# Kernel tuning notes

Measured on AMD Instinct MI355X. Metric: run time of the kernel, lower is better.

## Reference

```python
import math
import jax, jax.numpy as jnp
import numpy as np

THETA = 2 ** 16

def _get_freqs(n: int) -> jnp.ndarray:
    # positions quantized to multiples of 2 (pairs share a frequency)
    pos = jnp.floor(jnp.arange(n, dtype=jnp.float32) / 2.0) * 2.0
    return 1.0 / (THETA ** (pos / n)) / (2.0 * math.pi)  # (n,)

def _rope(phases: jnp.ndarray, v: jnp.ndarray) -> jnp.ndarray:
    # phases in 'cycles'; wrap to [0,1) then scale to radians
    ph = (phases % 1.0) * (2.0 * math.pi)
    c, s = jnp.cos(ph), jnp.sin(ph)
    # interleaved rotate-half: out[..., 2i] = -v[..., 2i+1], out[..., 2i+1] = v[..., 2i]
    v_rot = jnp.stack((-v[..., 1::2], v[..., ::2]), axis=-1).reshape(v.shape)
    return (v * c).astype(v.dtype) + (v_rot * s).astype(v.dtype)


def setup_inputs() -> dict:
    key = jax.random.key(0)
    kq, kv = jax.random.split(key)
    B, H, T, N, D = 2, 8, 2048, 1024, 128
    Q = jax.random.normal(kq, (B, H, T, N), dtype=jnp.float32)
    K = Q  # module asserts K is Q
    V = jax.random.normal(kv, (B, H, T, D), dtype=jnp.float32)
    return {"Q": Q, "K": K, "V": V}


def reference(Q, K, V):
    B, H, T, N = Q.shape
    freqs = _get_freqs(N)  # (N,)
    # r_phases: (T, N) = position * freq (broadcast over B, H)
    r_phases = jnp.arange(T, dtype=jnp.float32)[:, None] * freqs[None, :]
    QR = _rope(r_phases, Q)  # (B,H,T,N); KR = QR since K is Q
    scores = jnp.einsum('bhtn,bhsn->bhts', QR, QR)  # (B,H,T,T)
    causal = jnp.tril(jnp.ones((T, T), dtype=bool), k=-1)  # strict lower triangle
    scores = jnp.where(causal, scores, 0.0)
    return jnp.einsum('bhts,bhsd->bhtd', scores, V)  # (B,H,T,D)
```

## Files before the change

### kernel.cpp

```cpp
#include <hip/hip_runtime.h>

typedef __bf16 bf16_t;
typedef bf16_t bf16x8 __attribute__((ext_vector_type(8)));
typedef float f32x4 __attribute__((ext_vector_type(4)));
typedef unsigned short u16;
typedef unsigned int u32;

#define T_DIM 2048
#define N_DIM 1024
#define D_DIM 128

__device__ __forceinline__ u16 f32_to_bf16(float f) {
    u32 u = __builtin_bit_cast(u32, f);
    u += 0x7FFFu + ((u >> 16) & 1u);
    return (u16)(u >> 16);
}
__device__ __forceinline__ float bf16_to_f32(u16 v) {
    u32 u = (u32)v << 16;
    return __builtin_bit_cast(float, u);
}

typedef __attribute__((address_space(1))) const u32 guint;
typedef __attribute__((address_space(3))) u32 luint;
__device__ __forceinline__ void stage16(const void* g, void* l) {
    __builtin_amdgcn_global_load_lds((guint*)g, (luint*)l, 16, 0, 0);
}
__device__ __forceinline__ void wait_vm0_barrier() {
    asm volatile("s_waitcnt vmcnt(0)" ::: "memory");
    __builtin_amdgcn_s_barrier();
}

__global__ void ropet_kernel(const float* __restrict__ Q, u16* __restrict__ QR,
                             u16* __restrict__ QRt) {
    __shared__ __align__(16) u16 til[64][136];
    const int bh  = blockIdx.x >> 8;
    const int rem = blockIdx.x & 255;
    const int t0 = (rem >> 3) * 64, n0 = (rem & 7) * 128;
    const float* src = Q + (size_t)bh * ((size_t)T_DIM * N_DIM) + (size_t)t0 * N_DIM + n0;
    u16* qdst = QR + (size_t)bh * ((size_t)T_DIM * N_DIM) + (size_t)t0 * N_DIM + n0;
    #pragma unroll
    for (int k = 0; k < 4; ++k) {
        const int slot = k * 256 + threadIdx.x;
        const int r  = slot >> 4;
        const int f8 = slot & 15;
        const float4 qa = *(const float4*)(src + (size_t)r * N_DIM + f8 * 8);
        const float4 qb = *(const float4*)(src + (size_t)r * N_DIM + f8 * 8 + 4);
        const float vin[4][2] = {{qa.x, qa.y}, {qa.z, qa.w}, {qb.x, qb.y}, {qb.z, qb.w}};
        const int t = t0 + r;
        u16 ov[8];
        #pragma unroll
        for (int pp = 0; pp < 4; ++pp) {
            const int pidx = (n0 >> 1) + f8 * 4 + pp;
            const float freq = exp2f((float)pidx * (-1.0f / 32.0f)) * 0.15915494309189535f;
            float ph = (float)t * freq;
            ph -= floorf(ph);
            const float s = __builtin_amdgcn_sinf(ph);
            const float c = __builtin_amdgcn_cosf(ph);
            ov[2 * pp]     = f32_to_bf16(vin[pp][0] * c - vin[pp][1] * s);
            ov[2 * pp + 1] = f32_to_bf16(vin[pp][1] * c + vin[pp][0] * s);
        }
        *(uint4*)(qdst + (size_t)r * N_DIM + f8 * 8) = *(const uint4*)ov;
        *(uint4*)(&til[r][(f8 * 8) ^ (((r >> 3) & 7) << 3)]) = *(const uint4*)ov;
    }
    __syncthreads();
    u16* tdst = QRt + (size_t)bh * ((size_t)N_DIM * T_DIM) + (size_t)n0 * T_DIM + t0;
    #pragma unroll
    for (int k = 0; k < 4; ++k) {
        const int slot = k * 256 + threadIdx.x;
        const int nl = slot >> 3;
        const int t8 = slot & 7;
        u16 ov2[8];
        #pragma unroll
        for (int e = 0; e < 8; ++e)
            ov2[e] = til[t8 * 8 + e][nl ^ (t8 << 3)];
        *(uint4*)(tdst + (size_t)nl * T_DIM + t8 * 8) = *(const uint4*)ov2;
    }
}

__global__ void vt_kernel(const float* __restrict__ V, u16* __restrict__ Vt) {
    __shared__ u16 tile[64][65];
    const int bh   = blockIdx.x >> 6;
    const int rem  = blockIdx.x & 63;
    const int t0 = (rem >> 1) * 64, d0 = (rem & 1) * 64;
    const float* src = V + ((size_t)bh * T_DIM + t0) * D_DIM + d0;
    #pragma unroll
    for (int k = 0; k < 16; ++k) {
        int linear = k * 256 + threadIdx.x;
        int r = linear >> 6, c = linear & 63;
        tile[r][c] = f32_to_bf16(src[(size_t)r * D_DIM + c]);
    }
    __syncthreads();
    u16* dst = Vt + ((size_t)bh * D_DIM + d0) * T_DIM + t0;
    #pragma unroll
    for (int k = 0; k < 16; ++k) {
        int linear = k * 256 + threadIdx.x;
        int dr = linear >> 6, tc = linear & 63;
        dst[(size_t)dr * T_DIM + tc] = tile[tc][dr];
    }
}

__global__ __launch_bounds__(512, 2)
void statescan_kernel(const u16* __restrict__ QRt, const u16* __restrict__ Vt,
                      u16* __restrict__ UP) {
    __shared__ __align__(16) u16 Smem[24576];

    const int b  = blockIdx.x;
    const int bh = b >> 4;
    const int nt = (b >> 1) & 7;
    const int dt = b & 1;

    const int tid  = threadIdx.x;
    const int w    = tid >> 6;
    const int wy   = w >> 1, wx = w & 1;
    const int lane = tid & 63;
    const int quad = lane >> 4;
    const int l15  = lane & 15;
    const int sw   = l15 & 7;
    const int srow = lane >> 3;
    const int scol = (lane & 7) ^ (srow & 7);

    const u16* Ag = Vt  + (size_t)bh * ((size_t)D_DIM * T_DIM) + (size_t)(dt * 64)  * T_DIM;
    const u16* Bg = QRt + (size_t)bh * ((size_t)N_DIM * T_DIM) + (size_t)(nt * 128) * T_DIM;

    const f32x4 fz = {0.f, 0.f, 0.f, 0.f};
    f32x4 acc[4];
    #pragma unroll
    for (int nj = 0; nj < 4; ++nj) acc[nj] = fz;

    auto STAGE = [&](int buf, int s) {
        const int toff = s * 64;
        if (w < 4) {
            #pragma unroll
            for (int ia = 0; ia < 2; ++ia)
                stage16(Ag + (size_t)(w * 16 + ia * 8 + srow) * T_DIM + toff + scol * 8,
                        Smem + buf * 4096 + (w * 16 + ia * 8) * 64);
        }
        #pragma unroll
        for (int ib = 0; ib < 2; ++ib)
            stage16(Bg + (size_t)(w * 16 + ib * 8 + srow) * T_DIM + toff + scol * 8,
                    Smem + 8192 + buf * 8192 + (w * 16 + ib * 8) * 64);
    };

    u16* upb = UP + (size_t)(bh * 16) * (128 * (size_t)N_DIM)
                  + (size_t)(dt * 64) * N_DIM + nt * 128;

    auto WRITE_UP = [&](int ci) {
        u16* ub = upb + (size_t)ci * (128 * (size_t)N_DIM);
        #pragma unroll
        for (int nj = 0; nj < 4; ++nj)
            #pragma unroll
            for (int rr = 0; rr < 4; ++rr)
                ub[(size_t)(wy * 16 + quad * 4 + rr) * N_DIM + wx * 64 + nj * 16 + l15]
                    = f32_to_bf16(acc[nj][rr]);
    };

    STAGE(0, 0);
    wait_vm0_barrier();
    int buf = 0;
    for (int s = 0; s < 30; ++s) {
        if ((s & 1) == 0) WRITE_UP(s >> 1);
        if (s < 29) STAGE(buf ^ 1, s + 1);
        const char* As = (const char*)(Smem + buf * 4096);
        const char* Bs = (const char*)(Smem + 8192 + buf * 8192);
        #pragma unroll
        for (int kc = 0; kc < 2; ++kc) {
            bf16x8 af, bfr[4];
            af = *(const bf16x8*)(As + (wy * 16 + l15) * 128 + (((kc * 4 + quad) ^ sw) << 4));
            #pragma unroll
            for (int nj = 0; nj < 4; ++nj)
                bfr[nj] = *(const bf16x8*)(Bs + (wx * 64 + nj * 16 + l15) * 128 + (((kc * 4 + quad) ^ sw) << 4));
            #pragma unroll
            for (int nj = 0; nj < 4; ++nj)
                acc[nj] = __builtin_amdgcn_mfma_f32_16x16x32_bf16(af, bfr[nj], acc[nj], 0, 0, 0);
        }
        wait_vm0_barrier();
        buf ^= 1;
    }
    WRITE_UP(15);
}

__global__ __launch_bounds__(512, 2)
void attn3_kernel(const u16* __restrict__ QR, const u16* __restrict__ UP,
                  const u16* __restrict__ Vt, float* __restrict__ Out) {
    __shared__ __align__(16) u16 Smem[32768];
    u16 (*Ps)[140] = (u16 (*)[140])Smem;

    const int b  = (blockIdx.x & 7) * 32 + (blockIdx.x >> 3);
    const int bh = b >> 4;
    const int i  = b & 15;

    const int tid  = threadIdx.x;
    const int w    = tid >> 6;
    const int wy   = w >> 1, wx = w & 1;
    const int lane = tid & 63;
    const int quad = lane >> 4;
    const int l15  = lane & 15;
    const int sw   = l15 & 7;
    const int srow = lane >> 3;
    const int scol = (lane & 7) ^ (srow & 7);

    const u16* Ap = QR + (size_t)bh * ((size_t)T_DIM * N_DIM)
                       + (size_t)(i * 128 + w * 16 + srow) * N_DIM + scol * 8;
    const u16* Bp = UP + (size_t)(b * 128 + w * 16 + srow) * N_DIM + scol * 8;

    const f32x4 fz = {0.f, 0.f, 0.f, 0.f};
    f32x4 sm[2][4], si[2][4];
    #pragma unroll
    for (int mi = 0; mi < 2; ++mi)
        #pragma unroll
        for (int nj = 0; nj < 4; ++nj) {
            sm[mi][nj] = fz;
            si[mi][nj] = fz;
        }

    auto STAGE = [&](int buf, int kk16) {
        const int kk = kk16 * 64;
        #pragma unroll
        for (int ii = 0; ii < 2; ++ii) {
            stage16(Ap + (size_t)(ii * 8) * N_DIM + kk, Smem + buf * 8192 + (w * 16 + ii * 8) * 64);
            stage16(Bp + (size_t)(ii * 8) * N_DIM + kk, Smem + 16384 + buf * 8192 + (w * 16 + ii * 8) * 64);
        }
    };

    STAGE(0, 0);
    wait_vm0_barrier();
    int buf = 0;
    for (int kk16 = 0; kk16 < 16; ++kk16) {
        if (kk16 < 15) STAGE(buf ^ 1, kk16 + 1);
        const char* As = (const char*)(Smem + buf * 8192);
        const char* Bs = (const char*)(Smem + 16384 + buf * 8192);
        #pragma unroll
        for (int kc = 0; kc < 2; ++kc) {
            bf16x8 af[2], bm[4], bi[4];
            #pragma unroll
            for (int mi = 0; mi < 2; ++mi)
                af[mi] = *(const bf16x8*)(As + (wy * 32 + mi * 16 + l15) * 128 + (((kc * 4 + quad) ^ sw) << 4));
            #pragma unroll
            for (int nj = 0; nj < 4; ++nj) {
                bm[nj] = *(const bf16x8*)(Bs + (wx * 64 + nj * 16 + l15) * 128 + (((kc * 4 + quad) ^ sw) << 4));
                bi[nj] = *(const bf16x8*)(As + (wx * 64 + nj * 16 + l15) * 128 + (((kc * 4 + quad) ^ sw) << 4));
            }
            #pragma unroll
            for (int mi = 0; mi < 2; ++mi)
                #pragma unroll
                for (int nj = 0; nj < 4; ++nj) {
                    sm[mi][nj] = __builtin_amdgcn_mfma_f32_16x16x32_bf16(af[mi], bm[nj], sm[mi][nj], 0, 0, 0);
                    si[mi][nj] = __builtin_amdgcn_mfma_f32_16x16x32_bf16(af[mi], bi[nj], si[mi][nj], 0, 0, 0);
                }
        }
        wait_vm0_barrier();
        buf ^= 1;
    }

    #pragma unroll
    for (int mi = 0; mi < 2; ++mi) {
        const int rowb = wy * 32 + mi * 16 + quad * 4;
        #pragma unroll
        for (int nj = 0; nj < 4; ++nj) {
            const int col = wx * 64 + nj * 16 + l15;
            #pragma unroll
            for (int rr = 0; rr < 4; ++rr)
                if (col >= rowb + rr) si[mi][nj][rr] = 0.f;
        }
    }
    #pragma unroll
    for (int mi = 0; mi < 2; ++mi) {
        const int rowb = wy * 32 + mi * 16 + quad * 4;
        #pragma unroll
        for (int nj = 0; nj < 4; ++nj) {
            const int col = wx * 64 + nj * 16 + l15;
            #pragma unroll
            for (int rr = 0; rr < 4; ++rr)
                Ps[rowb + rr][col] = f32_to_bf16(si[mi][nj][rr]);
        }
    }
    __syncthreads();

    const u16* vjb = Vt + (size_t)bh * ((size_t)D_DIM * T_DIM)
                        + (size_t)(wx * 64 + l15) * T_DIM + i * 128 + quad * 8;
    #pragma unroll
    for (int kc = 0; kc < 4; ++kc) {
        bf16x8 pf[2];
        #pragma unroll
        for (int mi = 0; mi < 2; ++mi)
            pf[mi] = *(const bf16x8*)(&Ps[wy * 32 + mi * 16 + l15][kc * 32 + quad * 8]);
        #pragma unroll
        for (int nj = 0; nj < 4; ++nj) {
            const bf16x8 vv = *(const bf16x8*)(vjb + (size_t)(nj * 16) * T_DIM + kc * 32);
            #pragma unroll
            for (int mi = 0; mi < 2; ++mi)
                sm[mi][nj] = __builtin_amdgcn_mfma_f32_16x16x32_bf16(pf[mi], vv, sm[mi][nj], 0, 0, 0);
        }
    }

    float* ob = Out + ((size_t)bh * T_DIM + (size_t)i * 128) * D_DIM;
    #pragma unroll
    for (int mi = 0; mi < 2; ++mi)
        #pragma unroll
        for (int nj = 0; nj < 4; ++nj)
            #pragma unroll
            for (int rr = 0; rr < 4; ++rr)
                ob[(size_t)(wy * 32 + mi * 16 + quad * 4 + rr) * D_DIM + wx * 64 + nj * 16 + l15]
                    = sm[mi][nj][rr];
}

__global__ void rope_kernel(const float* __restrict__ Q, u16* __restrict__ QR) {
    const int g = blockIdx.x * 256 + threadIdx.x;
    const int base = g * 4;
    const int t  = (base >> 9) & (T_DIM - 1);
    const int p0 = base & 511;
    const float4 qa = ((const float4*)Q)[g * 2];
    const float4 qb = ((const float4*)Q)[g * 2 + 1];
    const float vin[4][2] = {{qa.x, qa.y}, {qa.z, qa.w}, {qb.x, qb.y}, {qb.z, qb.w}};
    u16 ov[8];
    #pragma unroll
    for (int uu = 0; uu < 4; ++uu) {
        const float freq = exp2f((float)(p0 + uu) * (-1.0f / 32.0f)) * 0.15915494309189535f;
        float ph = (float)t * freq;
        ph = ph - floorf(ph);
        const float s = __builtin_amdgcn_sinf(ph);
        const float c = __builtin_amdgcn_cosf(ph);
        ov[2 * uu]     = f32_to_bf16(vin[uu][0] * c - vin[uu][1] * s);
        ov[2 * uu + 1] = f32_to_bf16(vin[uu][1] * c + vin[uu][0] * s);
    }
    ((uint4*)QR)[g] = *(const uint4*)ov;
}

__device__ __forceinline__ int run_start(int b) { return b < 128 ? 5 * b : 640 + 4 * (b - 128); }

__global__ __launch_bounds__(256, 2)
void attn_kernel(const u16* __restrict__ QR, const u16* __restrict__ Vt,
                 float* __restrict__ Out, u16* __restrict__ Part) {
    __shared__ __align__(16) u16 Smem[17920];
    u16 (*As)[64]  = (u16 (*)[64])Smem;
    u16 (*Bs)[64]  = (u16 (*)[64])(Smem + 8192);
    u16 (*Ps)[140] = (u16 (*)[140])Smem;

    const int b     = blockIdx.x;
    const int start = run_start(b);
    const int len   = b < 128 ? 5 : 4;

    const int tid  = threadIdx.x;
    const int w    = tid >> 6;
    const int wy   = w >> 1, wx = w & 1;
    const int lane = tid & 63;
    const int quad = lane >> 4;
    const int l15  = lane & 15;
    const int sw   = l15 & 7;
    const int srow = lane >> 3;
    const int scol = (lane & 7) ^ (srow & 7);

    const f32x4 fz = {0.f, 0.f, 0.f, 0.f};
    f32x4 o_acc[4][4];
    int cur_bh = -1, cur_qt = -1;
    bool hasj0 = false;
    const u16* QRb = QR;
    const u16* Ap  = QR;
    const u16* Vb  = Vt;

    for (int it = 0; it < len; ++it) {
        const int i = start + it;
        const int bh = i / 136;
        const int r  = i - bh * 136;
        int qt = 15, j = 0, acc = 0;
        #pragma unroll 1
        for (int q = 0; q < 16; ++q) {
            if (r < acc + q + 1) { qt = q; j = r - acc; break; }
            acc += q + 1;
        }

        if (qt != cur_qt || bh != cur_bh) {
            if (cur_qt >= 0) {
                if (hasj0) {
                    float* ob = Out + ((size_t)cur_bh * T_DIM + (size_t)cur_qt * 128) * D_DIM;
                    #pragma unroll
                    for (int mi = 0; mi < 4; ++mi)
                        #pragma unroll
                        for (int nj = 0; nj < 4; ++nj)
                            #pragma unroll
                            for (int rr = 0; rr < 4; ++rr)
                                ob[(size_t)(wy * 64 + mi * 16 + quad * 4 + rr) * D_DIM + wx * 64 + nj * 16 + l15] = o_acc[mi][nj][rr];
                } else {
                    u16* pb = Part + (size_t)b * 16384;
                    #pragma unroll
                    for (int mi = 0; mi < 4; ++mi)
                        #pragma unroll
                        for (int nj = 0; nj < 4; ++nj)
                            #pragma unroll
                            for (int rr = 0; rr < 4; ++rr)
                                pb[(wy * 64 + mi * 16 + quad * 4 + rr) * 128 + wx * 64 + nj * 16 + l15] = f32_to_bf16(o_acc[mi][nj][rr]);
                }
            }
            cur_bh = bh; cur_qt = qt; hasj0 = (j == 0);
            #pragma unroll
            for (int mi = 0; mi < 4; ++mi)
                #pragma unroll
                for (int nj = 0; nj < 4; ++nj)
                    o_acc[mi][nj] = fz;
            QRb = QR + (size_t)bh * (T_DIM * N_DIM);
            Ap  = QRb + (size_t)(qt * 128 + w * 32 + srow) * N_DIM + scol * 8;
            Vb  = Vt + (size_t)bh * (D_DIM * T_DIM) + (size_t)(wx * 64 + l15) * T_DIM + quad * 8;
        }

        const u16* Bp = QRb + (size_t)(j * 128 + w * 32 + srow) * N_DIM + scol * 8;
        f32x4 s_acc[4][4];
        #pragma unroll
        for (int mi = 0; mi < 4; ++mi)
            #pragma unroll
            for (int nj = 0; nj < 4; ++nj)
                s_acc[mi][nj] = fz;

        __syncthreads();

        for (int kk = 0; kk < N_DIM; kk += 64) {
            #pragma unroll
            for (int ii = 0; ii < 4; ++ii) {
                stage16(Ap + (size_t)ii * 8 * N_DIM + kk, &As[w * 32 + ii * 8][0]);
                stage16(Bp + (size_t)ii * 8 * N_DIM + kk, &Bs[w * 32 + ii * 8][0]);
            }
            __syncthreads();
            #pragma unroll
            for (int kc = 0; kc < 2; ++kc) {
                bf16x8 af[4], bfr[4];
                #pragma unroll
                for (int mi = 0; mi < 4; ++mi)
                    af[mi] = *(const bf16x8*)((const char*)As + (wy * 64 + mi * 16 + l15) * 128 + (((kc * 4 + quad) ^ sw) << 4));
                #pragma unroll
                for (int nj = 0; nj < 4; ++nj)
                    bfr[nj] = *(const bf16x8*)((const char*)Bs + (wx * 64 + nj * 16 + l15) * 128 + (((kc * 4 + quad) ^ sw) << 4));
                #pragma unroll
                for (int mi = 0; mi < 4; ++mi)
                    #pragma unroll
                    for (int nj = 0; nj < 4; ++nj)
                        s_acc[mi][nj] = __builtin_amdgcn_mfma_f32_16x16x32_bf16(af[mi], bfr[nj], s_acc[mi][nj], 0, 0, 0);
            }
            __syncthreads();
        }

        if (j == qt) {
            #pragma unroll
            for (int mi = 0; mi < 4; ++mi) {
                const int rowb = wy * 64 + mi * 16 + quad * 4;
                #pragma unroll
                for (int nj = 0; nj < 4; ++nj) {
                    const int col = wx * 64 + nj * 16 + l15;
                    #pragma unroll
                    for (int rr = 0; rr < 4; ++rr)
                        if (col >= rowb + rr) s_acc[mi][nj][rr] = 0.f;
                }
            }
        }

        #pragma unroll
        for (int mi = 0; mi < 4; ++mi) {
            const int rowb = wy * 64 + mi * 16 + quad * 4;
            #pragma unroll
            for (int nj = 0; nj < 4; ++nj) {
                const int col = wx * 64 + nj * 16 + l15;
                #pragma unroll
                for (int rr = 0; rr < 4; ++rr)
                    Ps[rowb + rr][col] = f32_to_bf16(s_acc[mi][nj][rr]);
            }
        }
        __syncthreads();

        const u16* vjb = Vb + j * 128;
        #pragma unroll
        for (int kc = 0; kc < 4; ++kc) {
            bf16x8 pf[4];
            #pragma unroll
            for (int mi = 0; mi < 4; ++mi)
                pf[mi] = *(const bf16x8*)(&Ps[wy * 64 + mi * 16 + l15][kc * 32 + quad * 8]);
            #pragma unroll
            for (int nj = 0; nj < 4; ++nj) {
                const bf16x8 vv = *(const bf16x8*)(vjb + (size_t)(nj * 16) * T_DIM + kc * 32);
                #pragma unroll
                for (int mi = 0; mi < 4; ++mi)
                    o_acc[mi][nj] = __builtin_amdgcn_mfma_f32_16x16x32_bf16(pf[mi], vv, o_acc[mi][nj], 0, 0, 0);
            }
        }
    }

    if (hasj0) {
        float* ob = Out + ((size_t)cur_bh * T_DIM + (size_t)cur_qt * 128) * D_DIM;
        #pragma unroll
        for (int mi = 0; mi < 4; ++mi)
            #pragma unroll
            for (int nj = 0; nj < 4; ++nj)
                #pragma unroll
                for (int rr = 0; rr < 4; ++rr)
                    ob[(size_t)(wy * 64 + mi * 16 + quad * 4 + rr) * D_DIM + wx * 64 + nj * 16 + l15] = o_acc[mi][nj][rr];
    } else {
        u16* pb = Part + (size_t)b * 16384;
        #pragma unroll
        for (int mi = 0; mi < 4; ++mi)
            #pragma unroll
            for (int nj = 0; nj < 4; ++nj)
                #pragma unroll
                for (int rr = 0; rr < 4; ++rr)
                    pb[(wy * 64 + mi * 16 + quad * 4 + rr) * 128 + wx * 64 + nj * 16 + l15] = f32_to_bf16(o_acc[mi][nj][rr]);
    }
}

__global__ void combine_kernel(float* __restrict__ Out, const u16* __restrict__ Part) {
    const int bh = blockIdx.x & 15;
    const int qt = 1 + (blockIdx.x >> 4);
    const int ts = bh * 136 + (qt * (qt + 1)) / 2;
    const int lo = ts + 1, hi = ts + qt;
    int bmin = (lo <= 640) ? (lo + 4) / 5 : 128 + (lo - 640 + 3) / 4;
    int writers[4], nw = 0;
    for (int bb = bmin; bb < 512 && run_start(bb) <= hi && nw < 4; ++bb)
        writers[nw++] = bb;
    if (nw == 0) return;
    float* ob = Out + ((size_t)bh * T_DIM + (size_t)qt * 128) * D_DIM;
    const int tid = threadIdx.x;
    #pragma unroll 1
    for (int e = 0; e < 64; ++e) {
        const int idx = e * 256 + tid;
        float a = ob[idx];
        for (int k = 0; k < nw; ++k)
            a += bf16_to_f32(Part[(size_t)writers[k] * 16384 + idx]);
        ob[idx] = a;
    }
}

extern "C" void kernel_launch(void* const* d_in, const int* in_sizes, int n_in,
                              void* d_out, int out_size, void* d_ws, size_t ws_size,
                              hipStream_t stream) {
    const float* Q = (const float*)d_in[0];
    const float* V = (const float*)d_in[2];
    float* Out = (float*)d_out;

    const size_t QR_E = (size_t)16 * T_DIM * N_DIM;
    const size_t VT_E = (size_t)16 * D_DIM * T_DIM;
    const size_t UP_E = (size_t)256 * 128 * N_DIM;
    const size_t need = (QR_E * 2 + VT_E + UP_E) * 2;

    if (ws_size >= need) {
        u16* QRw  = (u16*)d_ws;
        u16* QRtw = QRw + QR_E;
        u16* Vtw  = QRtw + QR_E;
        u16* UPw  = Vtw + VT_E;

        ropet_kernel<<<dim3(4096), dim3(256), 0, stream>>>(Q, QRw, QRtw);
        vt_kernel<<<dim3(1024), dim3(256), 0, stream>>>(V, Vtw);
        statescan_kernel<<<dim3(256), dim3(512), 0, stream>>>(QRtw, Vtw, UPw);
        attn3_kernel<<<dim3(256), dim3(512), 0, stream>>>(QRw, UPw, Vtw, Out);
    } else {
        u16* QRw  = (u16*)d_ws;
        u16* Vtw  = QRw + QR_E;
        u16* Part = Vtw + VT_E;

        rope_kernel<<<dim3(16384), dim3(256), 0, stream>>>(Q, QRw);
        vt_kernel<<<dim3(1024), dim3(256), 0, stream>>>(V, Vtw);
        attn_kernel<<<dim3(512), dim3(256), 0, stream>>>(QRw, Vtw, Out, Part);
        combine_kernel<<<dim3(240), dim3(256), 0, stream>>>(Out, Part);
    }
}
```

Measured before the change: 362.9 us.

## Triple-buffer LDS staging in scan and attention kernels, enlarge rope-transpose tiles

Converts the statescan and attn3 main loops from double-buffered to triple-buffered global-to-LDS staging with partial vmcnt waits, so loads for two steps ahead overlap the MFMA work. A-tile staging in statescan is spread across all eight waves instead of four. Launch bounds drop to one block per CU because of the larger LDS use, and a barrier is added before the Ps write since Ps now aliases the staging buffers. The rope-transpose kernel processes 128-row tiles with half the blocks, to amortise per-block overhead.

New measurement: 360.5 us. Within noise of the previous version (-0.7%).

```diff
diff --git a/kernel.cpp b/kernel.cpp
--- a/kernel.cpp
+++ b/kernel.cpp
@@ -32,14 +32,14 @@
 
 __global__ void ropet_kernel(const float* __restrict__ Q, u16* __restrict__ QR,
                              u16* __restrict__ QRt) {
-    __shared__ __align__(16) u16 til[64][136];
-    const int bh  = blockIdx.x >> 8;
-    const int rem = blockIdx.x & 255;
-    const int t0 = (rem >> 3) * 64, n0 = (rem & 7) * 128;
+    __shared__ __align__(16) u16 til[128][136];
+    const int bh  = blockIdx.x >> 7;
+    const int rem = blockIdx.x & 127;
+    const int t0 = (rem >> 3) * 128, n0 = (rem & 7) * 128;
     const float* src = Q + (size_t)bh * ((size_t)T_DIM * N_DIM) + (size_t)t0 * N_DIM + n0;
     u16* qdst = QR + (size_t)bh * ((size_t)T_DIM * N_DIM) + (size_t)t0 * N_DIM + n0;
     #pragma unroll
-    for (int k = 0; k < 4; ++k) {
+    for (int k = 0; k < 8; ++k) {
         const int slot = k * 256 + threadIdx.x;
         const int r  = slot >> 4;
         const int f8 = slot & 15;
@@ -60,20 +60,20 @@
             ov[2 * pp + 1] = f32_to_bf16(vin[pp][1] * c + vin[pp][0] * s);
         }
         *(uint4*)(qdst + (size_t)r * N_DIM + f8 * 8) = *(const uint4*)ov;
-        *(uint4*)(&til[r][(f8 * 8) ^ (((r >> 3) & 7) << 3)]) = *(const uint4*)ov;
+        *(uint4*)(&til[r][(f8 * 8) ^ (((r >> 3) & 15) << 3)]) = *(const uint4*)ov;
     }
     __syncthreads();
     u16* tdst = QRt + (size_t)bh * ((size_t)N_DIM * T_DIM) + (size_t)n0 * T_DIM + t0;
     #pragma unroll
-    for (int k = 0; k < 4; ++k) {
+    for (int k = 0; k < 8; ++k) {
         const int slot = k * 256 + threadIdx.x;
-        const int nl = slot >> 3;
-        const int t8 = slot & 7;
+        const int nl = slot >> 4;
+        const int to = slot & 15;
         u16 ov2[8];
         #pragma unroll
         for (int e = 0; e < 8; ++e)
-            ov2[e] = til[t8 * 8 + e][nl ^ (t8 << 3)];
-        *(uint4*)(tdst + (size_t)nl * T_DIM + t8 * 8) = *(const uint4*)ov2;
+            ov2[e] = til[to * 8 + e][nl ^ (to << 3)];
+        *(uint4*)(tdst + (size_t)nl * T_DIM + to * 8) = *(const uint4*)ov2;
     }
 }
 
@@ -99,10 +99,10 @@
     }
 }
 
-__global__ __launch_bounds__(512, 2)
+__global__ __launch_bounds__(512, 1)
 void statescan_kernel(const u16* __restrict__ QRt, const u16* __restrict__ Vt,
                       u16* __restrict__ UP) {
-    __shared__ __align__(16) u16 Smem[24576];
+    __shared__ __align__(16) u16 Smem[36864];
 
     const int b  = blockIdx.x;
     const int bh = b >> 4;
@@ -127,18 +127,14 @@
     #pragma unroll
     for (int nj = 0; nj < 4; ++nj) acc[nj] = fz;
 
-    auto STAGE = [&](int buf, int s) {
+    auto STAGE = [&](int stg, int s) {
         const int toff = s * 64;
-        if (w < 4) {
-            #pragma unroll
-            for (int ia = 0; ia < 2; ++ia)
-                stage16(Ag + (size_t)(w * 16 + ia * 8 + srow) * T_DIM + toff + scol * 8,
-                        Smem + buf * 4096 + (w * 16 + ia * 8) * 64);
-        }
+        stage16(Ag + (size_t)(w * 8 + srow) * T_DIM + toff + scol * 8,
+                Smem + stg * 4096 + (w * 8) * 64);
         #pragma unroll
         for (int ib = 0; ib < 2; ++ib)
             stage16(Bg + (size_t)(w * 16 + ib * 8 + srow) * T_DIM + toff + scol * 8,
-                    Smem + 8192 + buf * 8192 + (w * 16 + ib * 8) * 64);
+                    Smem + 12288 + stg * 8192 + (w * 16 + ib * 8) * 64);
     };
 
     u16* upb = UP + (size_t)(bh * 16) * (128 * (size_t)N_DIM)
@@ -154,14 +150,9 @@
                     = f32_to_bf16(acc[nj][rr]);
     };
 
-    STAGE(0, 0);
-    wait_vm0_barrier();
-    int buf = 0;
-    for (int s = 0; s < 30; ++s) {
-        if ((s & 1) == 0) WRITE_UP(s >> 1);
-        if (s < 29) STAGE(buf ^ 1, s + 1);
-        const char* As = (const char*)(Smem + buf * 4096);
-        const char* Bs = (const char*)(Smem + 8192 + buf * 8192);
+    auto MFMA_STEP = [&](int stg) {
+        const char* As = (const char*)(Smem + stg * 4096);
+        const char* Bs = (const char*)(Smem + 12288 + stg * 8192);
         #pragma unroll
         for (int kc = 0; kc < 2; ++kc) {
             bf16x8 af, bfr[4];
@@ -173,16 +164,29 @@
             for (int nj = 0; nj < 4; ++nj)
                 acc[nj] = __builtin_amdgcn_mfma_f32_16x16x32_bf16(af, bfr[nj], acc[nj], 0, 0, 0);
         }
-        wait_vm0_barrier();
-        buf ^= 1;
-    }
+    };
+
+    STAGE(0, 0);
+    STAGE(1, 1);
+    int s0 = 0, s1 = 1, s2 = 2;
+    for (int s = 0; s < 29; ++s) {
+        asm volatile("s_waitcnt vmcnt(3)" ::: "memory");
+        __builtin_amdgcn_s_barrier();
+        if ((s & 1) == 0) WRITE_UP(s >> 1);
+        if (s < 28) STAGE(s2, s + 2);
+        MFMA_STEP(s0);
+        const int t = s0; s0 = s1; s1 = s2; s2 = t;
+    }
+    asm volatile("s_waitcnt vmcnt(0)" ::: "memory");
+    __builtin_amdgcn_s_barrier();
+    MFMA_STEP(s0);
     WRITE_UP(15);
 }
 
-__global__ __launch_bounds__(512, 2)
+__global__ __launch_bounds__(512, 1)
 void attn3_kernel(const u16* __restrict__ QR, const u16* __restrict__ UP,
                   const u16* __restrict__ Vt, float* __restrict__ Out) {
-    __shared__ __align__(16) u16 Smem[32768];
+    __shared__ __align__(16) u16 Smem[49152];
     u16 (*Ps)[140] = (u16 (*)[140])Smem;
 
     const int b  = (blockIdx.x & 7) * 32 + (blockIdx.x >> 3);
@@ -213,22 +217,18 @@
             si[mi][nj] = fz;
         }
 
-    auto STAGE = [&](int buf, int kk16) {
+    auto STAGE = [&](int stg, int kk16) {
         const int kk = kk16 * 64;
         #pragma unroll
         for (int ii = 0; ii < 2; ++ii) {
-            stage16(Ap + (size_t)(ii * 8) * N_DIM + kk, Smem + buf * 8192 + (w * 16 + ii * 8) * 64);
-            stage16(Bp + (size_t)(ii * 8) * N_DIM + kk, Smem + 16384 + buf * 8192 + (w * 16 + ii * 8) * 64);
+            stage16(Ap + (size_t)(ii * 8) * N_DIM + kk, Smem + stg * 8192 + (w * 16 + ii * 8) * 64);
+            stage16(Bp + (size_t)(ii * 8) * N_DIM + kk, Smem + 24576 + stg * 8192 + (w * 16 + ii * 8) * 64);
         }
     };
 
-    STAGE(0, 0);
-    wait_vm0_barrier();
-    int buf = 0;
-    for (int kk16 = 0; kk16 < 16; ++kk16) {
-        if (kk16 < 15) STAGE(buf ^ 1, kk16 + 1);
-        const char* As = (const char*)(Smem + buf * 8192);
-        const char* Bs = (const char*)(Smem + 16384 + buf * 8192);
+    auto MFMA_STEP = [&](int stg) {
+        const char* As = (const char*)(Smem + stg * 8192);
+        const char* Bs = (const char*)(Smem + 24576 + stg * 8192);
         #pragma unroll
         for (int kc = 0; kc < 2; ++kc) {
             bf16x8 af[2], bm[4], bi[4];
@@ -248,9 +248,21 @@
                     si[mi][nj] = __builtin_amdgcn_mfma_f32_16x16x32_bf16(af[mi], bi[nj], si[mi][nj], 0, 0, 0);
                 }
         }
-        wait_vm0_barrier();
-        buf ^= 1;
-    }
+    };
+
+    STAGE(0, 0);
+    STAGE(1, 1);
+    int s0 = 0, s1 = 1, s2 = 2;
+    for (int k = 0; k < 15; ++k) {
+        asm volatile("s_waitcnt vmcnt(4)" ::: "memory");
+        __builtin_amdgcn_s_barrier();
+        if (k < 14) STAGE(s2, k + 2);
+        MFMA_STEP(s0);
+        const int t = s0; s0 = s1; s1 = s2; s2 = t;
+    }
+    asm volatile("s_waitcnt vmcnt(0)" ::: "memory");
+    __builtin_amdgcn_s_barrier();
+    MFMA_STEP(s0);
 
     #pragma unroll
     for (int mi = 0; mi < 2; ++mi) {
@@ -263,6 +275,7 @@
                 if (col >= rowb + rr) si[mi][nj][rr] = 0.f;
         }
     }
+    __syncthreads();
     #pragma unroll
     for (int mi = 0; mi < 2; ++mi) {
         const int rowb = wy * 32 + mi * 16 + quad * 4;
@@ -542,7 +555,7 @@
         u16* Vtw  = QRtw + QR_E;
         u16* UPw  = Vtw + VT_E;
 
-        ropet_kernel<<<dim3(4096), dim3(256), 0, stream>>>(Q, QRw, QRtw);
+        ropet_kernel<<<dim3(2048), dim3(256), 0, stream>>>(Q, QRw, QRtw);
         vt_kernel<<<dim3(1024), dim3(256), 0, stream>>>(V, Vtw);
         statescan_kernel<<<dim3(256), dim3(512), 0, stream>>>(QRtw, Vtw, UPw);
         attn3_kernel<<<dim3(256), dim3(512), 0, stream>>>(QRw, UPw, Vtw, Out);
```
